# Kernel tuning notes

Measured on AMD Instinct MI355X. Metric: run time of the kernel, lower is better.

## Reference

```python
import jax, jax.numpy as jnp
import numpy as np

SEQ, BATCH, IN, HID = 1024, 64, 512, 1024

def setup_inputs() -> dict:
    key = jax.random.key(0)
    k1, k2, k3, k4, k5 = jax.random.split(key, 5)
    bound = 1.0 / np.sqrt(HID)
    return {
        "inputs": jax.random.normal(k1, (SEQ, BATCH, IN), dtype=jnp.float32),
        "W_ih": jax.random.uniform(k2, (HID, IN), minval=-bound, maxval=bound, dtype=jnp.float32),
        "W_hh": jax.random.uniform(k3, (HID, HID), minval=-bound, maxval=bound, dtype=jnp.float32),
        "b_ih": jax.random.uniform(k4, (HID,), minval=-bound, maxval=bound, dtype=jnp.float32),
        "b_hh": jax.random.uniform(k5, (HID,), minval=-bound, maxval=bound, dtype=jnp.float32),
    }

def reference(inputs, W_ih, W_hh, b_ih, b_hh):
    # Precompute input projections for all timesteps in one GEMM: [S,B,H]
    x_proj = jnp.einsum('sbi,hi->sbh', inputs, W_ih) + b_ih + b_hh
    h0 = jnp.zeros((inputs.shape[1], W_hh.shape[0]), dtype=inputs.dtype)

    def step(h, xp):
        h_new = jnp.tanh(xp + h @ W_hh.T)  # tanh RNNCell
        return h_new, h_new

    _, hiddens = jax.lax.scan(step, h0, x_proj)
    return hiddens  # [S, B, H]
```

## Files before the change

kernel.cpp:

```cpp
#include <hip/hip_runtime.h>
#include <hip/hip_bf16.h>

#define SEQ   1024
#define BATCH 64
#define INDIM 512
#define HID   1024

typedef __attribute__((ext_vector_type(8))) short bf16x8;
typedef __attribute__((ext_vector_type(4))) float f32x4;
typedef __attribute__((ext_vector_type(4))) int   i32x4;

static __device__ __forceinline__ short f2bf(float f) {
    union { float f; unsigned u; } v; v.f = f;
    unsigned u = v.u;
    unsigned r = u + 0x7fffu + ((u >> 16) & 1u);
    return (short)(r >> 16);
}

static __device__ __forceinline__ i32x4 load16_coherent(const void* p) {
    i32x4 r;
    asm volatile("global_load_dwordx4 %0, %1, off sc0 sc1" : "=v"(r) : "v"(p) : "memory");
    return r;
}

static __device__ __forceinline__ float fast_tanh(float x) {
    x = fminf(9.0f, fmaxf(-9.0f, x));
    float e = __builtin_amdgcn_exp2f(2.8853900817779268f * x);
    return (e - 1.0f) * __builtin_amdgcn_rcpf(e + 1.0f);
}

__global__ __launch_bounds__(256) void cvt8_kernel(const float* __restrict__ src,
                                                   short* __restrict__ dst, int n8) {
    int i = blockIdx.x * blockDim.x + threadIdx.x;
    int stride = gridDim.x * blockDim.x;
    for (; i < n8; i += stride) {
        const float* s = src + (size_t)i * 8;
        float4 lo = *reinterpret_cast<const float4*>(s);
        float4 hi = *reinterpret_cast<const float4*>(s + 4);
        bf16x8 v;
        v[0] = f2bf(lo.x); v[1] = f2bf(lo.y); v[2] = f2bf(lo.z); v[3] = f2bf(lo.w);
        v[4] = f2bf(hi.x); v[5] = f2bf(hi.y); v[6] = f2bf(hi.z); v[7] = f2bf(hi.w);
        *reinterpret_cast<bf16x8*>(dst + (size_t)i * 8) = v;
    }
}

__global__ __launch_bounds__(256) void proj_kernel(
    const float* __restrict__ x,
    const short* __restrict__ wih,
    const float* __restrict__ b_ih,
    const float* __restrict__ b_hh,
    float* __restrict__ out)
{
    const int tid  = threadIdx.x;
    const int lane = tid & 63;
    const int w    = tid >> 6;
    const int wm   = w & 1, wn = w >> 1;
    const int l15  = lane & 15;
    const int quad = lane >> 4;

    const int id  = blockIdx.x;
    const int xcd = id & 7;
    const int q   = id >> 3;
    const int n   = q & 15;
    const int p   = (q >> 4) * 8 + xcd;

    const int bm = p * 64 + wm * 32;
    const int bn = n * 64 + wn * 32;

    f32x4 acc[2][2] = {};

    for (int kk = 0; kk < INDIM; kk += 32) {
        const int kbase = kk + quad * 8;
        bf16x8 a[2], b[2];
#pragma unroll
        for (int mi = 0; mi < 2; ++mi) {
            const float* ap = x + (size_t)(bm + mi * 16 + l15) * INDIM + kbase;
            float4 lo = *reinterpret_cast<const float4*>(ap);
            float4 hi = *reinterpret_cast<const float4*>(ap + 4);
            bf16x8 af;
            af[0] = f2bf(lo.x); af[1] = f2bf(lo.y); af[2] = f2bf(lo.z); af[3] = f2bf(lo.w);
            af[4] = f2bf(hi.x); af[5] = f2bf(hi.y); af[6] = f2bf(hi.z); af[7] = f2bf(hi.w);
            a[mi] = af;
        }
#pragma unroll
        for (int ni = 0; ni < 2; ++ni)
            b[ni] = *reinterpret_cast<const bf16x8*>(wih + (size_t)(bn + ni * 16 + l15) * INDIM + kbase);
#pragma unroll
        for (int mi = 0; mi < 2; ++mi)
#pragma unroll
            for (int ni = 0; ni < 2; ++ni)
                acc[mi][ni] = __builtin_amdgcn_mfma_f32_16x16x32_bf16(a[mi], b[ni], acc[mi][ni], 0, 0, 0);
    }

#pragma unroll
    for (int mi = 0; mi < 2; ++mi) {
#pragma unroll
        for (int ni = 0; ni < 2; ++ni) {
            const int col = bn + ni * 16 + l15;
            const float bias = b_ih[col] + b_hh[col];
#pragma unroll
            for (int reg = 0; reg < 4; ++reg) {
                const int row = bm + mi * 16 + quad * 4 + reg;
                out[(size_t)row * HID + col] = acc[mi][ni][reg] + bias;
            }
        }
    }
}

__global__ __launch_bounds__(256) void proj_kernel_bf2(
    const short* __restrict__ xbf,
    const short* __restrict__ wih,
    const float* __restrict__ b_ih,
    const float* __restrict__ b_hh,
    float* __restrict__ out)
{
    const int tid  = threadIdx.x;
    const int lane = tid & 63;
    const int w    = tid >> 6;
    const int wm   = w & 1, wn = w >> 1;
    const int l15  = lane & 15;
    const int quad = lane >> 4;

    const int id  = blockIdx.x;
    const int xcd = id & 7;
    const int q   = id >> 3;
    const int n   = q & 7;
    const int p   = (q >> 3) * 8 + xcd;

    const int bm = p * 128 + wm * 64;
    const int bn = n * 128 + wn * 64;

    f32x4 acc[4][4] = {};

    for (int kk = 0; kk < INDIM; kk += 32) {
        const int kbase = kk + quad * 8;
        bf16x8 a[4], b[4];
#pragma unroll
        for (int mi = 0; mi < 4; ++mi)
            a[mi] = *reinterpret_cast<const bf16x8*>(xbf + (size_t)(bm + mi * 16 + l15) * INDIM + kbase);
#pragma unroll
        for (int ni = 0; ni < 4; ++ni)
            b[ni] = *reinterpret_cast<const bf16x8*>(wih + (size_t)(bn + ni * 16 + l15) * INDIM + kbase);
#pragma unroll
        for (int mi = 0; mi < 4; ++mi)
#pragma unroll
            for (int ni = 0; ni < 4; ++ni)
                acc[mi][ni] = __builtin_amdgcn_mfma_f32_16x16x32_bf16(a[mi], b[ni], acc[mi][ni], 0, 0, 0);
    }

#pragma unroll
    for (int mi = 0; mi < 4; ++mi) {
#pragma unroll
        for (int ni = 0; ni < 4; ++ni) {
            const int col = bn + ni * 16 + l15;
            const float bias = b_ih[col] + b_hh[col];
#pragma unroll
            for (int reg = 0; reg < 4; ++reg) {
                const int row = bm + mi * 16 + quad * 4 + reg;
                out[(size_t)row * HID + col] = acc[mi][ni][reg] + bias;
            }
        }
    }
}

__global__ __launch_bounds__(256) void rnn_scan_kernel(
    float* __restrict__ out,
    const short* __restrict__ whh,
    short* __restrict__ hb0,
    short* __restrict__ hb1,
    unsigned int* __restrict__ flags)
{
    const int tid  = threadIdx.x;
    const int lane = tid & 63;
    const int w    = tid >> 6;
    const int l15  = lane & 15;
    const int quad = lane >> 4;

    const int gid = blockIdx.x;
    const int g   = gid >> 4;
    const int r   = gid & 15;
    const int b0  = g * 16;
    const int n0  = r * 64;

    bf16x8 wfrag[4][8];
#pragma unroll
    for (int nt = 0; nt < 4; ++nt)
#pragma unroll
        for (int ks = 0; ks < 8; ++ks) {
            const int k = 256 * w + ks * 32 + quad * 8;
            wfrag[nt][ks] = *reinterpret_cast<const bf16x8*>(
                whh + (size_t)(n0 + nt * 16 + l15) * HID + k);
        }

    __shared__ float red[4 * 1024];

    short* hbufs[2] = { hb0, hb1 };
    unsigned int* gflags = flags + g * 64;
    const unsigned int* wflag = gflags + w * 4;

    const int m  = tid >> 4;
    const int c0 = (tid & 15) * 4;

    for (int t = 0; t < SEQ; ++t) {
        const short* hc = hbufs[t & 1];
        short*       hn = hbufs[(t + 1) & 1];

        const size_t oidx = (size_t)t * (BATCH * HID) + (size_t)(b0 + m) * HID + n0 + c0;
        float4 xp = *reinterpret_cast<const float4*>(out + oidx);

        if (t != 0) {
            const unsigned tgt = (unsigned)t;
            for (;;) {
                i32x4 fl;
                asm volatile("global_load_dwordx4 %0, %1, off sc0 sc1\n\ts_waitcnt vmcnt(0)"
                             : "=v"(fl) : "v"(wflag) : "memory");
                if ((unsigned)fl[0] >= tgt && (unsigned)fl[1] >= tgt &&
                    (unsigned)fl[2] >= tgt && (unsigned)fl[3] >= tgt) break;
            }
        }

        i32x4 araw[8];
        const short* abase = hc + (size_t)(b0 + l15) * HID + 256 * w + quad * 8;
#pragma unroll
        for (int ks = 0; ks < 8; ++ks)
            araw[ks] = load16_coherent(abase + ks * 32);

        f32x4 acc[4] = {};
        asm volatile("s_waitcnt vmcnt(4)"
            : "+v"(araw[0]), "+v"(araw[1]), "+v"(araw[2]), "+v"(araw[3]) :: "memory");
#pragma unroll
        for (int ks = 0; ks < 4; ++ks) {
            bf16x8 a = __builtin_bit_cast(bf16x8, araw[ks]);
#pragma unroll
            for (int nt = 0; nt < 4; ++nt)
                acc[nt] = __builtin_amdgcn_mfma_f32_16x16x32_bf16(a, wfrag[nt][ks], acc[nt], 0, 0, 0);
        }
        asm volatile("s_waitcnt vmcnt(0)"
            : "+v"(araw[4]), "+v"(araw[5]), "+v"(araw[6]), "+v"(araw[7]) :: "memory");
#pragma unroll
        for (int ks = 4; ks < 8; ++ks) {
            bf16x8 a = __builtin_bit_cast(bf16x8, araw[ks]);
#pragma unroll
            for (int nt = 0; nt < 4; ++nt)
                acc[nt] = __builtin_amdgcn_mfma_f32_16x16x32_bf16(a, wfrag[nt][ks], acc[nt], 0, 0, 0);
        }

#pragma unroll
        for (int nt = 0; nt < 4; ++nt)
#pragma unroll
            for (int reg = 0; reg < 4; ++reg)
                red[w * 1024 + (quad * 4 + reg) * 64 + nt * 16 + l15] = acc[nt][reg];
        __syncthreads();

        {
            f32x4 s = *reinterpret_cast<const f32x4*>(&red[0 * 1024 + m * 64 + c0]);
#pragma unroll
            for (int wk = 1; wk < 4; ++wk) {
                f32x4 sp = *reinterpret_cast<const f32x4*>(&red[wk * 1024 + m * 64 + c0]);
                s[0] += sp[0]; s[1] += sp[1]; s[2] += sp[2]; s[3] += sp[3];
            }

            float v0 = fast_tanh(s[0] + xp.x);
            float v1 = fast_tanh(s[1] + xp.y);
            float v2 = fast_tanh(s[2] + xp.z);
            float v3 = fast_tanh(s[3] + xp.w);
            *reinterpret_cast<float4*>(out + oidx) = make_float4(v0, v1, v2, v3);

            unsigned lo = (unsigned)(unsigned short)f2bf(v0) | ((unsigned)(unsigned short)f2bf(v1) << 16);
            unsigned hi = (unsigned)(unsigned short)f2bf(v2) | ((unsigned)(unsigned short)f2bf(v3) << 16);
            unsigned long long pk = (unsigned long long)lo | ((unsigned long long)hi << 32);
            __hip_atomic_store(
                reinterpret_cast<unsigned long long*>(hn + (size_t)(b0 + m) * HID + n0 + c0),
                pk, __ATOMIC_RELAXED, __HIP_MEMORY_SCOPE_AGENT);
        }

        __syncthreads();
        if (tid == 0) {
            __builtin_amdgcn_fence(__ATOMIC_RELEASE, "agent");
            __hip_atomic_store(&gflags[r], (unsigned)(t + 1),
                               __ATOMIC_RELAXED, __HIP_MEMORY_SCOPE_AGENT);
        }
    }
}

extern "C" void kernel_launch(void* const* d_in, const int* in_sizes, int n_in,
                              void* d_out, int out_size, void* d_ws, size_t ws_size,
                              hipStream_t stream) {
    const float* x    = (const float*)d_in[0];
    const float* wih  = (const float*)d_in[1];
    const float* whh  = (const float*)d_in[2];
    const float* b_ih = (const float*)d_in[3];
    const float* b_hh = (const float*)d_in[4];
    float* out = (float*)d_out;

    char* ws = (char*)d_ws;
    unsigned int* flags = (unsigned int*)(ws + 0);
    short* hb0    = (short*)(ws + 4096);
    short* hb1    = (short*)(ws + 4096 + 131072);
    short* wih_bf = (short*)(ws + 266240);
    short* whh_bf = (short*)(ws + 1314816);
    short* x_bf   = (short*)(ws + 3411968);
    const size_t ws_needed_xbf = 3411968ull + (size_t)SEQ * BATCH * INDIM * 2;

    hipMemsetAsync(d_ws, 0, 266240, stream);

    cvt8_kernel<<<256, 256, 0, stream>>>(wih, wih_bf, HID * INDIM / 8);
    cvt8_kernel<<<512, 256, 0, stream>>>(whh, whh_bf, HID * HID / 8);

    if (ws_size >= ws_needed_xbf) {
        cvt8_kernel<<<2048, 256, 0, stream>>>(x, x_bf, SEQ * BATCH * INDIM / 8);
        proj_kernel_bf2<<<4096, 256, 0, stream>>>(x_bf, wih_bf, b_ih, b_hh, out);
    } else {
        proj_kernel<<<16384, 256, 0, stream>>>(x, wih_bf, b_ih, b_hh, out);
    }

    void* args[] = { (void*)&out, (void*)&whh_bf, (void*)&hb0, (void*)&hb1, (void*)&flags };
    hipLaunchCooperativeKernel((const void*)rnn_scan_kernel, dim3(64), dim3(256),
                               args, 0, stream);
}
```

Measured before the change: 4.854 ms.

## Replace flag-based barrier with timestep-tagged hidden-state packets in RNN scan

Measured after the change: 4.343 ms. 1.12x faster.

```diff
diff --git a/kernel.cpp b/kernel.cpp
--- a/kernel.cpp
+++ b/kernel.cpp
@@ -15,12 +15,6 @@
     unsigned u = v.u;
     unsigned r = u + 0x7fffu + ((u >> 16) & 1u);
     return (short)(r >> 16);
-}
-
-static __device__ __forceinline__ i32x4 load16_coherent(const void* p) {
-    i32x4 r;
-    asm volatile("global_load_dwordx4 %0, %1, off sc0 sc1" : "=v"(r) : "v"(p) : "memory");
-    return r;
 }
 
 static __device__ __forceinline__ float fast_tanh(float x) {
@@ -163,12 +157,11 @@
     }
 }
 
-__global__ __launch_bounds__(256) void rnn_scan_kernel(
+__global__ __launch_bounds__(256) void rnn_scan_tag_kernel(
     float* __restrict__ out,
     const short* __restrict__ whh,
-    short* __restrict__ hb0,
-    short* __restrict__ hb1,
-    unsigned int* __restrict__ flags)
+    unsigned int* __restrict__ hbt0,
+    unsigned int* __restrict__ hbt1)
 {
     const int tid  = threadIdx.x;
     const int lane = tid & 63;
@@ -192,71 +185,70 @@
                 whh + (size_t)(n0 + nt * 16 + l15) * HID + k);
         }
 
-    __shared__ float red[4 * 1024];
-
-    short* hbufs[2] = { hb0, hb1 };
-    unsigned int* gflags = flags + g * 64;
-    const unsigned int* wflag = gflags + w * 4;
+    __shared__ float red[2][4096];
+
+    unsigned int* hbufs[2] = { hbt0, hbt1 };
 
     const int m  = tid >> 4;
     const int c0 = (tid & 15) * 4;
 
     for (int t = 0; t < SEQ; ++t) {
-        const short* hc = hbufs[t & 1];
-        short*       hn = hbufs[(t + 1) & 1];
+        const unsigned int* hc = hbufs[t & 1];
+        unsigned int*       hn = hbufs[(t + 1) & 1];
 
         const size_t oidx = (size_t)t * (BATCH * HID) + (size_t)(b0 + m) * HID + n0 + c0;
         float4 xp = *reinterpret_cast<const float4*>(out + oidx);
 
-        if (t != 0) {
-            const unsigned tgt = (unsigned)t;
-            for (;;) {
-                i32x4 fl;
-                asm volatile("global_load_dwordx4 %0, %1, off sc0 sc1\n\ts_waitcnt vmcnt(0)"
-                             : "=v"(fl) : "v"(wflag) : "memory");
-                if ((unsigned)fl[0] >= tgt && (unsigned)fl[1] >= tgt &&
-                    (unsigned)fl[2] >= tgt && (unsigned)fl[3] >= tgt) break;
-            }
-        }
-
-        i32x4 araw[8];
-        const short* abase = hc + (size_t)(b0 + l15) * HID + 256 * w + quad * 8;
-#pragma unroll
-        for (int ks = 0; ks < 8; ++ks)
-            araw[ks] = load16_coherent(abase + ks * 32);
+        const char* pb = (const char*)hc +
+            (((size_t)(b0 + l15) * 256 + 64 * w + 2 * quad) << 4);
+        i32x4 sl[16];
+        int iter = 0;
+        for (;;) {
+#define PL(i, OFF) asm volatile("global_load_dwordx4 %0, %1, off offset:" OFF " sc0 sc1" \
+                                : "=v"(sl[i]) : "v"(pb) : "memory")
+            PL(0, "0");   PL(1, "16");  PL(2, "128"); PL(3, "144");
+            PL(4, "256"); PL(5, "272"); PL(6, "384"); PL(7, "400");
+            PL(8, "512"); PL(9, "528"); PL(10, "640"); PL(11, "656");
+            PL(12, "768"); PL(13, "784"); PL(14, "896"); PL(15, "912");
+#undef PL
+            asm volatile("s_waitcnt vmcnt(0)"
+                : "+v"(sl[0]), "+v"(sl[1]), "+v"(sl[2]), "+v"(sl[3]),
+                  "+v"(sl[4]), "+v"(sl[5]), "+v"(sl[6]), "+v"(sl[7]),
+                  "+v"(sl[8]), "+v"(sl[9]), "+v"(sl[10]), "+v"(sl[11]),
+                  "+v"(sl[12]), "+v"(sl[13]), "+v"(sl[14]), "+v"(sl[15]) :: "memory");
+            int ok = (sl[0][0] == t) & (sl[1][0] == t) & (sl[2][0] == t) & (sl[3][0] == t) &
+                     (sl[4][0] == t) & (sl[5][0] == t) & (sl[6][0] == t) & (sl[7][0] == t) &
+                     (sl[8][0] == t) & (sl[9][0] == t) & (sl[10][0] == t) & (sl[11][0] == t) &
+                     (sl[12][0] == t) & (sl[13][0] == t) & (sl[14][0] == t) & (sl[15][0] == t);
+            if (__all(ok)) break;
+            if (++iter >= 8192) break;
+        }
 
         f32x4 acc[4] = {};
-        asm volatile("s_waitcnt vmcnt(4)"
-            : "+v"(araw[0]), "+v"(araw[1]), "+v"(araw[2]), "+v"(araw[3]) :: "memory");
-#pragma unroll
-        for (int ks = 0; ks < 4; ++ks) {
-            bf16x8 a = __builtin_bit_cast(bf16x8, araw[ks]);
+#pragma unroll
+        for (int ks = 0; ks < 8; ++ks) {
+            i32x4 aw;
+            aw[0] = sl[2 * ks][2];     aw[1] = sl[2 * ks][3];
+            aw[2] = sl[2 * ks + 1][2]; aw[3] = sl[2 * ks + 1][3];
+            bf16x8 a = __builtin_bit_cast(bf16x8, aw);
 #pragma unroll
             for (int nt = 0; nt < 4; ++nt)
                 acc[nt] = __builtin_amdgcn_mfma_f32_16x16x32_bf16(a, wfrag[nt][ks], acc[nt], 0, 0, 0);
         }
-        asm volatile("s_waitcnt vmcnt(0)"
-            : "+v"(araw[4]), "+v"(araw[5]), "+v"(araw[6]), "+v"(araw[7]) :: "memory");
-#pragma unroll
-        for (int ks = 4; ks < 8; ++ks) {
-            bf16x8 a = __builtin_bit_cast(bf16x8, araw[ks]);
-#pragma unroll
-            for (int nt = 0; nt < 4; ++nt)
-                acc[nt] = __builtin_amdgcn_mfma_f32_16x16x32_bf16(a, wfrag[nt][ks], acc[nt], 0, 0, 0);
-        }
-
+
+        float* rw = &red[t & 1][0];
 #pragma unroll
         for (int nt = 0; nt < 4; ++nt)
 #pragma unroll
             for (int reg = 0; reg < 4; ++reg)
-                red[w * 1024 + (quad * 4 + reg) * 64 + nt * 16 + l15] = acc[nt][reg];
+                rw[w * 1024 + (quad * 4 + reg) * 64 + nt * 16 + l15] = acc[nt][reg];
         __syncthreads();
 
         {
-            f32x4 s = *reinterpret_cast<const f32x4*>(&red[0 * 1024 + m * 64 + c0]);
+            f32x4 s = *reinterpret_cast<const f32x4*>(&rw[m * 64 + c0]);
 #pragma unroll
             for (int wk = 1; wk < 4; ++wk) {
-                f32x4 sp = *reinterpret_cast<const f32x4*>(&red[wk * 1024 + m * 64 + c0]);
+                f32x4 sp = *reinterpret_cast<const f32x4*>(&rw[wk * 1024 + m * 64 + c0]);
                 s[0] += sp[0]; s[1] += sp[1]; s[2] += sp[2]; s[3] += sp[3];
             }
 
@@ -268,17 +260,11 @@
 
             unsigned lo = (unsigned)(unsigned short)f2bf(v0) | ((unsigned)(unsigned short)f2bf(v1) << 16);
             unsigned hi = (unsigned)(unsigned short)f2bf(v2) | ((unsigned)(unsigned short)f2bf(v3) << 16);
-            unsigned long long pk = (unsigned long long)lo | ((unsigned long long)hi << 32);
-            __hip_atomic_store(
-                reinterpret_cast<unsigned long long*>(hn + (size_t)(b0 + m) * HID + n0 + c0),
-                pk, __ATOMIC_RELAXED, __HIP_MEMORY_SCOPE_AGENT);
-        }
-
-        __syncthreads();
-        if (tid == 0) {
-            __builtin_amdgcn_fence(__ATOMIC_RELEASE, "agent");
-            __hip_atomic_store(&gflags[r], (unsigned)(t + 1),
-                               __ATOMIC_RELAXED, __HIP_MEMORY_SCOPE_AGENT);
+            i32x4 st;
+            st[0] = t + 1; st[1] = 0; st[2] = (int)lo; st[3] = (int)hi;
+            unsigned int* dst = hn + (((size_t)(b0 + m) * 256 + r * 16 + (tid & 15)) << 2);
+            asm volatile("global_store_dwordx4 %0, %1, off sc0 sc1"
+                         :: "v"(dst), "v"(st) : "memory");
         }
     }
 }
@@ -294,15 +280,14 @@
     float* out = (float*)d_out;
 
     char* ws = (char*)d_ws;
-    unsigned int* flags = (unsigned int*)(ws + 0);
-    short* hb0    = (short*)(ws + 4096);
-    short* hb1    = (short*)(ws + 4096 + 131072);
-    short* wih_bf = (short*)(ws + 266240);
-    short* whh_bf = (short*)(ws + 1314816);
-    short* x_bf   = (short*)(ws + 3411968);
-    const size_t ws_needed_xbf = 3411968ull + (size_t)SEQ * BATCH * INDIM * 2;
-
-    hipMemsetAsync(d_ws, 0, 266240, stream);
+    unsigned int* hbt0 = (unsigned int*)(ws + 0);
+    unsigned int* hbt1 = (unsigned int*)(ws + 262144);
+    short* wih_bf = (short*)(ws + 524288);
+    short* whh_bf = (short*)(ws + 1572864);
+    short* x_bf   = (short*)(ws + 3670016);
+    const size_t ws_needed_xbf = 3670016ull + (size_t)SEQ * BATCH * INDIM * 2;
+
+    hipMemsetAsync(d_ws, 0, 262144, stream);
 
     cvt8_kernel<<<256, 256, 0, stream>>>(wih, wih_bf, HID * INDIM / 8);
     cvt8_kernel<<<512, 256, 0, stream>>>(whh, whh_bf, HID * HID / 8);
@@ -314,7 +299,10 @@
         proj_kernel<<<16384, 256, 0, stream>>>(x, wih_bf, b_ih, b_hh, out);
     }
 
-    void* args[] = { (void*)&out, (void*)&whh_bf, (void*)&hb0, (void*)&hb1, (void*)&flags };
-    hipLaunchCooperativeKernel((const void*)rnn_scan_kernel, dim3(64), dim3(256),
-                               args, 0, stream);
-}
+    void* args[] = { (void*)&out, (void*)&whh_bf, (void*)&hbt0, (void*)&hbt1 };
+    hipError_t e = hipLaunchCooperativeKernel((const void*)rnn_scan_tag_kernel,
+                                              dim3(64), dim3(256), args, 0, stream);
+    if (e != hipSuccess) {
+        rnn_scan_tag_kernel<<<dim3(64), dim3(256), 0, stream>>>(out, whh_bf, hbt0, hbt1);
+    }
+}
```
